# Optimization experiments

Measured on AMD Instinct MI355X. Metric: run time of the kernel, lower is better.

The kernel has to match this reference:

```python
import jax, jax.numpy as jnp
import numpy as np

B, I, O = 4096, 2048, 2048
U_R, THR_MIN = 0.01, 0.01


def setup_inputs() -> dict:
    key = jax.random.key(0)
    ks = jax.random.split(key, 4)
    # Random small-scale weights (the module's ones-init saturates sigmoids;
    # math is identical, this just keeps values in a testable range).
    return {
        "x_t": jax.random.normal(ks[0], (B, I), jnp.float32),
        "u_t": jnp.zeros((B, O), jnp.float32),
        "b_t": jnp.zeros((B, O), jnp.float32),
        "spk": jnp.zeros((B, O), jnp.float32),
        "W_syn": jax.random.normal(ks[1], (O, I), jnp.float32) * 0.02,
        "b_syn": jnp.zeros((O,), jnp.float32),
        "W_Tm": jax.random.normal(ks[2], (O, O), jnp.float32) * 0.02,
        "b_Tm": jnp.zeros((O,), jnp.float32),
        "W_Tadp": jax.random.normal(ks[3], (O, O), jnp.float32) * 0.02,
        "b_Tadp": jnp.zeros((O,), jnp.float32),
    }


def reference(x_t, u_t, b_t, spk, W_syn, b_syn, W_Tm, b_Tm, W_Tadp, b_Tadp):
    # L1 = syn(x_t); Linear stores weight [out,in]
    L1 = x_t @ W_syn.T + b_syn                      # [B, O]
    alpha = jax.nn.sigmoid((L1 + u_t) @ W_Tm.T + b_Tm)
    rho = jax.nn.sigmoid((L1 + b_t) @ W_Tadp.T + b_Tadp)
    b_new = rho * b_t + (1.0 - rho) * spk
    thr = THR_MIN + 1.8 * b_new
    u_new = u_t + (-u_t + L1) / alpha
    o_spk = (u_new - thr > 0).astype(jnp.float32)
    # (state u_t would be reset via o_spk, but forward returns only spikes)
    return o_spk
```

## Files before the change

kernel.cpp:

```cpp
#include <hip/hip_runtime.h>
#include <cmath>

#define B_DIM 4096
#define O_DIM 2048
#define I_DIM 2048

typedef _Float16 f16x8 __attribute__((ext_vector_type(8)));
typedef float f32x4 __attribute__((ext_vector_type(4)));
typedef unsigned int uint;
typedef unsigned short ushort;

#define WSCALE   64.0f
#define WDESCALE 0.015625f
#define MBYTE    ((size_t)1024 * 1024)


__device__ __forceinline__ int TP(int r, int s) {
    return r * 16 + (((s ^ ((r >> 1) & 3))) << 2);
}

__device__ __forceinline__ float h2f(ushort u) {
    _Float16 h = __builtin_bit_cast(_Float16, u);
    return (float)h;
}

__device__ __forceinline__ void gload16(const uint* src, uint* lds) {
    __builtin_amdgcn_global_load_lds(
        (const __attribute__((address_space(1))) void*)src,
        (__attribute__((address_space(3))) void*)lds, 16, 0, 0);
}

__device__ __forceinline__ void split8(const float4 a, const float4 b,
                                       uint4& hi, uint4& lo) {
    auto h0 = __builtin_amdgcn_cvt_pkrtz(a.x, a.y);
    auto h1 = __builtin_amdgcn_cvt_pkrtz(a.z, a.w);
    auto h2 = __builtin_amdgcn_cvt_pkrtz(b.x, b.y);
    auto h3 = __builtin_amdgcn_cvt_pkrtz(b.z, b.w);
    auto l0 = __builtin_amdgcn_cvt_pkrtz(a.x - (float)h0[0], a.y - (float)h0[1]);
    auto l1 = __builtin_amdgcn_cvt_pkrtz(a.z - (float)h1[0], a.w - (float)h1[1]);
    auto l2 = __builtin_amdgcn_cvt_pkrtz(b.x - (float)h2[0], b.y - (float)h2[1]);
    auto l3 = __builtin_amdgcn_cvt_pkrtz(b.z - (float)h3[0], b.w - (float)h3[1]);
    hi.x = __builtin_bit_cast(uint, h0); hi.y = __builtin_bit_cast(uint, h1);
    hi.z = __builtin_bit_cast(uint, h2); hi.w = __builtin_bit_cast(uint, h3);
    lo.x = __builtin_bit_cast(uint, l0); lo.y = __builtin_bit_cast(uint, l1);
    lo.z = __builtin_bit_cast(uint, l2); lo.w = __builtin_bit_cast(uint, l3);
}

__device__ __forceinline__ float4 add4(const float4 a, const float4 b) {
    return make_float4(a.x + b.x, a.y + b.y, a.z + b.z, a.w + b.w);
}
__device__ __forceinline__ float4 mul64(const float4 a) {
    return make_float4(a.x * WSCALE, a.y * WSCALE, a.z * WSCALE, a.w * WSCALE);
}
__device__ __forceinline__ void unpack8(const uint4 h, const uint4 l,
                                        float4& f0, float4& f1) {
    f0.x = h2f((ushort)(h.x & 0xffff)) + h2f((ushort)(l.x & 0xffff));
    f0.y = h2f((ushort)(h.x >> 16))    + h2f((ushort)(l.x >> 16));
    f0.z = h2f((ushort)(h.y & 0xffff)) + h2f((ushort)(l.y & 0xffff));
    f0.w = h2f((ushort)(h.y >> 16))    + h2f((ushort)(l.y >> 16));
    f1.x = h2f((ushort)(h.z & 0xffff)) + h2f((ushort)(l.z & 0xffff));
    f1.y = h2f((ushort)(h.z >> 16))    + h2f((ushort)(l.z >> 16));
    f1.z = h2f((ushort)(h.w & 0xffff)) + h2f((ushort)(l.w & 0xffff));
    f1.w = h2f((ushort)(h.w >> 16))    + h2f((ushort)(l.w >> 16));
}

__global__ __launch_bounds__(256)
void prep(const float* __restrict__ x, const float* __restrict__ Wsyn,
          const float* __restrict__ WTm,
          const float* __restrict__ u, const float* __restrict__ b,
          const float* __restrict__ s,
          ushort* __restrict__ Xh, ushort* __restrict__ Xl,
          ushort* __restrict__ Wsh, ushort* __restrict__ Wsl,
          ushort* __restrict__ Mhp, uint* __restrict__ flag, int doX) {
    const uint NX = (uint)((size_t)B_DIM * I_DIM / 8);
    const uint NW = (uint)((size_t)O_DIM * I_DIM / 8);
    const uint NZ = (uint)((size_t)B_DIM * O_DIM / 8);
    const uint nx = doX ? NX : 0;
    const uint total = nx + 2 * NW + NZ;
    const uint stride = gridDim.x * blockDim.x;
    bool nz = false;
    for (uint t = blockIdx.x * blockDim.x + threadIdx.x; t < total; t += stride) {
        if (t < nx) {
            const size_t i = (size_t)t * 8;
            uint4 h, l;
            split8(*(const float4*)(x + i), *(const float4*)(x + i + 4), h, l);
            *(uint4*)(Xh + i) = h; *(uint4*)(Xl + i) = l;
        } else if (t < nx + NW) {
            const size_t i = (size_t)(t - nx) * 8;
            uint4 h, l;
            split8(mul64(*(const float4*)(Wsyn + i)),
                   mul64(*(const float4*)(Wsyn + i + 4)), h, l);
            *(uint4*)(Wsh + i) = h; *(uint4*)(Wsl + i) = l;
        } else if (t < nx + 2 * NW) {
            const size_t i = (size_t)(t - nx - NW) * 8;
            const float4 a = mul64(*(const float4*)(WTm + i));
            const float4 c = mul64(*(const float4*)(WTm + i + 4));
            auto h0 = __builtin_amdgcn_cvt_pkrtz(a.x, a.y);
            auto h1 = __builtin_amdgcn_cvt_pkrtz(a.z, a.w);
            auto h2 = __builtin_amdgcn_cvt_pkrtz(c.x, c.y);
            auto h3 = __builtin_amdgcn_cvt_pkrtz(c.z, c.w);
            uint4 h;
            h.x = __builtin_bit_cast(uint, h0); h.y = __builtin_bit_cast(uint, h1);
            h.z = __builtin_bit_cast(uint, h2); h.w = __builtin_bit_cast(uint, h3);
            *(uint4*)(Mhp + i) = h;
        } else {
            const size_t i = (size_t)(t - nx - 2 * NW) * 8;
            const float4 a0 = *(const float4*)(u + i), a1 = *(const float4*)(u + i + 4);
            const float4 b0 = *(const float4*)(b + i), b1 = *(const float4*)(b + i + 4);
            const float4 c0 = *(const float4*)(s + i), c1 = *(const float4*)(s + i + 4);
            nz |= (a0.x != 0.f) | (a0.y != 0.f) | (a0.z != 0.f) | (a0.w != 0.f);
            nz |= (a1.x != 0.f) | (a1.y != 0.f) | (a1.z != 0.f) | (a1.w != 0.f);
            nz |= (b0.x != 0.f) | (b0.y != 0.f) | (b0.z != 0.f) | (b0.w != 0.f);
            nz |= (b1.x != 0.f) | (b1.y != 0.f) | (b1.z != 0.f) | (b1.w != 0.f);
            nz |= (c0.x != 0.f) | (c0.y != 0.f) | (c0.z != 0.f) | (c0.w != 0.f);
            nz |= (c1.x != 0.f) | (c1.y != 0.f) | (c1.z != 0.f) | (c1.w != 0.f);
        }
    }
    if (nz) atomicOr(flag, 1u);
}

__global__ __launch_bounds__(1024)
void gemm1_d(const ushort* __restrict__ Xh, const ushort* __restrict__ Xl,
             const ushort* __restrict__ Wh, const ushort* __restrict__ Wl,
             const float* __restrict__ bias,
             ushort* __restrict__ Lh, ushort* __restrict__ Ll) {
    __shared__ uint S[3][12288];

    const int tid = threadIdx.x;
    const int lane = tid & 63;
    const int wid = tid >> 6;
    const int wm = wid >> 3;
    const int wn = wid & 7;

    int sid = blockIdx.x;
    sid = (sid & 7) * 32 + (sid >> 3);
    const int bx = sid & 7, by = sid >> 3;
    const int row0 = by * 128, col0 = bx * 256;

    const uint* src[3];
    int dbase[3];
#pragma unroll
    for (int i = 0; i < 3; i++) {
        const int ch = wid * 3 + i;
        const ushort* plane;
        int local, pbase, grow0;
        if (ch < 8)       { plane = Xh; local = ch;      pbase = 0;    grow0 = row0; }
        else if (ch < 16) { plane = Xl; local = ch - 8;  pbase = 2048; grow0 = row0; }
        else if (ch < 32) { plane = Wh; local = ch - 16; pbase = 4096; grow0 = col0; }
        else              { plane = Wl; local = ch - 32; pbase = 8192; grow0 = col0; }
        const int g = local * 64 + lane;
        const int r = g >> 2, q = (g & 3) ^ ((r >> 1) & 3);
        dbase[i] = pbase + local * 256;
        src[i] = (const uint*)plane + (size_t)(grow0 + r) * 1024 + q * 4;
    }

    f32x4 acc[4][2];
#pragma unroll
    for (int i = 0; i < 4; i++)
#pragma unroll
        for (int j = 0; j < 2; j++)
#pragma unroll
            for (int r = 0; r < 4; r++) acc[i][j][r] = 0.0f;

    const int fr = lane & 15;
    const int sl = lane >> 4;
    const int NT = I_DIM / 32;

#pragma unroll
    for (int i = 0; i < 3; i++) gload16(src[i], &S[0][dbase[i]]);
#pragma unroll
    for (int i = 0; i < 3; i++) gload16(src[i] + 16, &S[1][dbase[i]]);

    for (int t = 0; t < NT; t++) {
        if (t + 1 < NT) {
            asm volatile("s_waitcnt vmcnt(3)" ::: "memory");
        } else {
            asm volatile("s_waitcnt vmcnt(0)" ::: "memory");
        }
        asm volatile("s_barrier" ::: "memory");
        if (t + 2 < NT) {
            const int ko = (t + 2) * 16;
            uint* Sd = &S[(t + 2) % 3][0];
#pragma unroll
            for (int i = 0; i < 3; i++) gload16(src[i] + ko, &Sd[dbase[i]]);
        }
        const uint* Sc = &S[t % 3][0];
        f16x8 ah_[4], al_[4], bh_[2], bl_[2];
#pragma unroll
        for (int mi = 0; mi < 4; mi++) {
            const int r = wm * 64 + mi * 16 + fr;
            ah_[mi] = *(const f16x8*)&Sc[TP(r, sl)];
            al_[mi] = *(const f16x8*)&Sc[2048 + TP(r, sl)];
        }
#pragma unroll
        for (int ni = 0; ni < 2; ni++) {
            const int r = wn * 32 + ni * 16 + fr;
            bh_[ni] = *(const f16x8*)&Sc[4096 + TP(r, sl)];
            bl_[ni] = *(const f16x8*)&Sc[8192 + TP(r, sl)];
        }
#pragma unroll
        for (int mi = 0; mi < 4; mi++)
#pragma unroll
            for (int ni = 0; ni < 2; ni++) {
                acc[mi][ni] = __builtin_amdgcn_mfma_f32_16x16x32_f16(ah_[mi], bh_[ni], acc[mi][ni], 0, 0, 0);
                acc[mi][ni] = __builtin_amdgcn_mfma_f32_16x16x32_f16(ah_[mi], bl_[ni], acc[mi][ni], 0, 0, 0);
                acc[mi][ni] = __builtin_amdgcn_mfma_f32_16x16x32_f16(al_[mi], bh_[ni], acc[mi][ni], 0, 0, 0);
            }
    }

#pragma unroll
    for (int ni = 0; ni < 2; ni++) {
        const int col = col0 + wn * 32 + ni * 16 + fr;
        const float bv = bias[col];
#pragma unroll
        for (int mi = 0; mi < 4; mi++) {
            const int rb = row0 + wm * 64 + mi * 16 + ((lane >> 4) << 2);
            float e[4];
#pragma unroll
            for (int r = 0; r < 4; r++) e[r] = acc[mi][ni][r] * WDESCALE + bv;
            auto hp0 = __builtin_amdgcn_cvt_pkrtz(e[0], e[1]);
            auto hp1 = __builtin_amdgcn_cvt_pkrtz(e[2], e[3]);
            auto lp0 = __builtin_amdgcn_cvt_pkrtz(e[0] - (float)hp0[0], e[1] - (float)hp0[1]);
            auto lp1 = __builtin_amdgcn_cvt_pkrtz(e[2] - (float)hp1[0], e[3] - (float)hp1[1]);
            const uint uh0 = __builtin_bit_cast(uint, hp0);
            const uint uh1 = __builtin_bit_cast(uint, hp1);
            const uint ul0 = __builtin_bit_cast(uint, lp0);
            const uint ul1 = __builtin_bit_cast(uint, lp1);
            Lh[(size_t)(rb + 0) * O_DIM + col] = (ushort)(uh0 & 0xffff);
            Lh[(size_t)(rb + 1) * O_DIM + col] = (ushort)(uh0 >> 16);
            Lh[(size_t)(rb + 2) * O_DIM + col] = (ushort)(uh1 & 0xffff);
            Lh[(size_t)(rb + 3) * O_DIM + col] = (ushort)(uh1 >> 16);
            Ll[(size_t)(rb + 0) * O_DIM + col] = (ushort)(ul0 & 0xffff);
            Ll[(size_t)(rb + 1) * O_DIM + col] = (ushort)(ul0 >> 16);
            Ll[(size_t)(rb + 2) * O_DIM + col] = (ushort)(ul1 & 0xffff);
            Ll[(size_t)(rb + 3) * O_DIM + col] = (ushort)(ul1 >> 16);
        }
    }
}

__global__ __launch_bounds__(256)
void gemm1_b(const float* __restrict__ X,
             const ushort* __restrict__ Wh, const ushort* __restrict__ Wl,
             const float* __restrict__ bias,
             ushort* __restrict__ Lh, ushort* __restrict__ Ll) {
    __shared__ uint S[8192];

    const int tid = threadIdx.x;
    const int lane = tid & 63;
    const int wid = tid >> 6;
    const int wm = wid >> 1, wn = wid & 1;

    int sid = blockIdx.x;
    sid = (sid & 7) * 64 + (sid >> 3);
    const int bx = sid & 15, by = sid >> 4;
    const int row0 = by * 128, col0 = bx * 128;

    const int sr = tid >> 1;
    const int kh = (tid & 1) * 16;
    const int s0 = (tid & 1) * 2;
    const float* pA = X + (size_t)(row0 + sr) * I_DIM + kh;

    int r0, q0, r1, q1;
    {
        const int g0 = (wid * 2 + 0) * 64 + lane;
        const int g1 = (wid * 2 + 1) * 64 + lane;
        r0 = g0 >> 2; q0 = (g0 & 3) ^ ((r0 >> 1) & 3);
        r1 = g1 >> 2; q1 = (g1 & 3) ^ ((r1 >> 1) & 3);
    }
    const uint* sWh0 = (const uint*)Wh + (size_t)(col0 + r0) * 1024 + q0 * 4;
    const uint* sWh1 = (const uint*)Wh + (size_t)(col0 + r1) * 1024 + q1 * 4;
    const uint* sWl0 = (const uint*)Wl + (size_t)(col0 + r0) * 1024 + q0 * 4;
    const uint* sWl1 = (const uint*)Wl + (size_t)(col0 + r1) * 1024 + q1 * 4;
    const int c0 = (wid * 2 + 0) << 8;
    const int c1 = (wid * 2 + 1) << 8;

    f32x4 acc[4][4];
#pragma unroll
    for (int i = 0; i < 4; i++)
#pragma unroll
        for (int j = 0; j < 4; j++)
#pragma unroll
            for (int r = 0; r < 4; r++) acc[i][j][r] = 0.0f;

    const int fr = lane & 15;
    const int sl = lane >> 4;
    const int NT = I_DIM / 32;

    float4 a0 = *(const float4*)(pA + 0), a1 = *(const float4*)(pA + 4);
    float4 a2 = *(const float4*)(pA + 8), a3 = *(const float4*)(pA + 12);
    uint4 xh0, xl0, xh1, xl1;
    split8(a0, a1, xh0, xl0);
    split8(a2, a3, xh1, xl1);

    for (int t = 0; t < NT; t++) {
        __syncthreads();
        *(uint4*)&S[TP(sr, s0)] = xh0;         *(uint4*)&S[TP(sr, s0 + 1)] = xh1;
        *(uint4*)&S[2048 + TP(sr, s0)] = xl0;  *(uint4*)&S[2048 + TP(sr, s0 + 1)] = xl1;
        const int ko = t * 16;
        gload16(sWh0 + ko, &S[4096 + c0]);  gload16(sWh1 + ko, &S[4096 + c1]);
        gload16(sWl0 + ko, &S[6144 + c0]);  gload16(sWl1 + ko, &S[6144 + c1]);
        __syncthreads();
        if (t + 1 < NT) {
            const float* nA = pA + (t + 1) * 32;
            a0 = *(const float4*)(nA + 0); a1 = *(const float4*)(nA + 4);
            a2 = *(const float4*)(nA + 8); a3 = *(const float4*)(nA + 12);
        }
        f16x8 ah_[4], al_[4], bh_[4], bl_[4];
#pragma unroll
        for (int mi = 0; mi < 4; mi++) {
            const int r = wm * 64 + mi * 16 + fr;
            ah_[mi] = *(const f16x8*)&S[TP(r, sl)];
            al_[mi] = *(const f16x8*)&S[2048 + TP(r, sl)];
        }
#pragma unroll
        for (int ni = 0; ni < 4; ni++) {
            const int r = wn * 64 + ni * 16 + fr;
            bh_[ni] = *(const f16x8*)&S[4096 + TP(r, sl)];
            bl_[ni] = *(const f16x8*)&S[6144 + TP(r, sl)];
        }
#pragma unroll
        for (int mi = 0; mi < 4; mi++)
#pragma unroll
            for (int ni = 0; ni < 4; ni++) {
                acc[mi][ni] = __builtin_amdgcn_mfma_f32_16x16x32_f16(ah_[mi], bh_[ni], acc[mi][ni], 0, 0, 0);
                acc[mi][ni] = __builtin_amdgcn_mfma_f32_16x16x32_f16(ah_[mi], bl_[ni], acc[mi][ni], 0, 0, 0);
                acc[mi][ni] = __builtin_amdgcn_mfma_f32_16x16x32_f16(al_[mi], bh_[ni], acc[mi][ni], 0, 0, 0);
            }
        if (t + 1 < NT) {
            split8(a0, a1, xh0, xl0);
            split8(a2, a3, xh1, xl1);
        }
    }

    const int fr2 = lane & 15;
#pragma unroll
    for (int ni = 0; ni < 4; ni++) {
        const int col = col0 + wn * 64 + ni * 16 + fr2;
        const float bv = bias[col];
#pragma unroll
        for (int mi = 0; mi < 4; mi++) {
            const int rb = row0 + wm * 64 + mi * 16 + ((lane >> 4) << 2);
            float e[4];
#pragma unroll
            for (int r = 0; r < 4; r++) e[r] = acc[mi][ni][r] * WDESCALE + bv;
            auto hp0 = __builtin_amdgcn_cvt_pkrtz(e[0], e[1]);
            auto hp1 = __builtin_amdgcn_cvt_pkrtz(e[2], e[3]);
            auto lp0 = __builtin_amdgcn_cvt_pkrtz(e[0] - (float)hp0[0], e[1] - (float)hp0[1]);
            auto lp1 = __builtin_amdgcn_cvt_pkrtz(e[2] - (float)hp1[0], e[3] - (float)hp1[1]);
            const uint uh0 = __builtin_bit_cast(uint, hp0);
            const uint uh1 = __builtin_bit_cast(uint, hp1);
            const uint ul0 = __builtin_bit_cast(uint, lp0);
            const uint ul1 = __builtin_bit_cast(uint, lp1);
            Lh[(size_t)(rb + 0) * O_DIM + col] = (ushort)(uh0 & 0xffff);
            Lh[(size_t)(rb + 1) * O_DIM + col] = (ushort)(uh0 >> 16);
            Lh[(size_t)(rb + 2) * O_DIM + col] = (ushort)(uh1 & 0xffff);
            Lh[(size_t)(rb + 3) * O_DIM + col] = (ushort)(uh1 >> 16);
            Ll[(size_t)(rb + 0) * O_DIM + col] = (ushort)(ul0 & 0xffff);
            Ll[(size_t)(rb + 1) * O_DIM + col] = (ushort)(ul0 >> 16);
            Ll[(size_t)(rb + 2) * O_DIM + col] = (ushort)(ul1 & 0xffff);
            Ll[(size_t)(rb + 3) * O_DIM + col] = (ushort)(ul1 >> 16);
        }
    }
}

__global__ __launch_bounds__(256)
void stage2_fast(const ushort* __restrict__ Lhp, const ushort* __restrict__ Llp,
                 const ushort* __restrict__ Mhp,
                 const float* __restrict__ bTm, float* __restrict__ out,
                 const uint* __restrict__ flag,
                 uint* __restrict__ cnt, uint* __restrict__ list, uint cap) {
    if (*flag != 0) return;

    __shared__ uint S[3][4096];

    const int tid = threadIdx.x;
    const int lane = tid & 63;
    const int wid = tid >> 6;
    const int wm = wid >> 1, wn = wid & 1;

    int sid = blockIdx.x;
    sid = (sid & 7) * 64 + (sid >> 3);
    const int bx = sid & 15, by = sid >> 4;
    const int row0 = by * 128, col0 = bx * 128;

    const uint* srcL0; const uint* srcL1; const uint* srcM0; const uint* srcM1;
    {
        const int g0 = (wid * 2 + 0) * 64 + lane;
        const int g1 = (wid * 2 + 1) * 64 + lane;
        const int r0 = g0 >> 2, q0 = (g0 & 3) ^ ((r0 >> 1) & 3);
        const int r1 = g1 >> 2, q1 = (g1 & 3) ^ ((r1 >> 1) & 3);
        srcL0 = (const uint*)Lhp + (size_t)(row0 + r0) * 1024 + q0 * 4;
        srcL1 = (const uint*)Lhp + (size_t)(row0 + r1) * 1024 + q1 * 4;
        srcM0 = (const uint*)Mhp + (size_t)(col0 + r0) * 1024 + q0 * 4;
        srcM1 = (const uint*)Mhp + (size_t)(col0 + r1) * 1024 + q1 * 4;
    }
    const int c0 = (wid * 2 + 0) << 8;
    const int c1 = (wid * 2 + 1) << 8;

    f32x4 acc[4][4];
#pragma unroll
    for (int i = 0; i < 4; i++)
#pragma unroll
        for (int j = 0; j < 4; j++)
#pragma unroll
            for (int r = 0; r < 4; r++) acc[i][j][r] = 0.0f;

    const int fr = lane & 15;
    const int sl = lane >> 4;
    const int NT = O_DIM / 32;

    gload16(srcL0, &S[0][c0]);         gload16(srcL1, &S[0][c1]);
    gload16(srcM0, &S[0][2048 + c0]);  gload16(srcM1, &S[0][2048 + c1]);
    gload16(srcL0 + 16, &S[1][c0]);        gload16(srcL1 + 16, &S[1][c1]);
    gload16(srcM0 + 16, &S[1][2048 + c0]); gload16(srcM1 + 16, &S[1][2048 + c1]);

    for (int t = 0; t < NT; t++) {
        if (t + 1 < NT) {
            asm volatile("s_waitcnt vmcnt(4)" ::: "memory");
        } else {
            asm volatile("s_waitcnt vmcnt(0)" ::: "memory");
        }
        asm volatile("s_barrier" ::: "memory");
        if (t + 2 < NT) {
            const int ko = (t + 2) * 16;
            uint* Sd = &S[(t + 2) % 3][0];
            gload16(srcL0 + ko, &Sd[c0]);         gload16(srcL1 + ko, &Sd[c1]);
            gload16(srcM0 + ko, &Sd[2048 + c0]);  gload16(srcM1 + ko, &Sd[2048 + c1]);
        }
        const uint* Sc = &S[t % 3][0];
        f16x8 lh_[4], mh_[4];
#pragma unroll
        for (int mi = 0; mi < 4; mi++)
            lh_[mi] = *(const f16x8*)&Sc[TP(wm * 64 + mi * 16 + fr, sl)];
#pragma unroll
        for (int ni = 0; ni < 4; ni++)
            mh_[ni] = *(const f16x8*)&Sc[2048 + TP(wn * 64 + ni * 16 + fr, sl)];
#pragma unroll
        for (int mi = 0; mi < 4; mi++)
#pragma unroll
            for (int ni = 0; ni < 4; ni++)
                acc[mi][ni] = __builtin_amdgcn_mfma_f32_16x16x32_f16(lh_[mi], mh_[ni], acc[mi][ni], 0, 0, 0);
    }
    __syncthreads();

    float* Sf = (float*)&S[0][0];
    float bmv[4];
#pragma unroll
    for (int ni = 0; ni < 4; ni++)
        bmv[ni] = bTm[col0 + wn * 64 + ni * 16 + fr];

    const int erow = tid >> 1;
    const int ecg  = tid & 1;

#pragma unroll
    for (int h = 0; h < 2; h++) {
        if (h) __syncthreads();
#pragma unroll
        for (int ni2 = 0; ni2 < 2; ni2++) {
            const int ni = h * 2 + ni2;
#pragma unroll
            for (int mi = 0; mi < 4; mi++) {
                const int rbL = wm * 64 + mi * 16 + ((lane >> 4) << 2);
#pragma unroll
                for (int r = 0; r < 4; r++) {
                    const int row = rbL + r;
                    const int cm = wn * 32 + ni2 * 16 + fr;
                    const int phys = (cm + ((row >> 2) & 3) * 16 + (row & 3) * 4) & 63;
                    Sf[row * 64 + phys] = acc[mi][ni][r] * WDESCALE + bmv[ni];
                }
            }
        }
        __syncthreads();
        const int rsw = ((erow >> 2) & 3) * 16 + (erow & 3) * 4;
        float z[32];
#pragma unroll
        for (int j = 0; j < 8; j++) {
            const int phys = (ecg * 32 + j * 4 + rsw) & 63;
            *(float4*)&z[j * 4] = *(const float4*)&Sf[erow * 64 + phys];
        }
        const int colBase = col0 + ecg * 64 + h * 32;
        const size_t idx0 = (size_t)(row0 + erow) * O_DIM + colBase;
        uint4 lh4[4], ll4[4];
#pragma unroll
        for (int j = 0; j < 4; j++) {
            lh4[j] = ((const uint4*)(Lhp + idx0))[j];
            ll4[j] = ((const uint4*)(Llp + idx0))[j];
        }
        float ov[32];
#pragma unroll
        for (int m = 0; m < 32; m++) {
            const uint hu = ((const uint*)lh4)[m >> 1];
            const uint lu = ((const uint*)ll4)[m >> 1];
            const ushort hs = (m & 1) ? (ushort)(hu >> 16) : (ushort)(hu & 0xffff);
            const ushort ls = (m & 1) ? (ushort)(lu >> 16) : (ushort)(lu & 0xffff);
            const float l1 = h2f(hs) + h2f(ls);
            const float zm = z[m];
            const float ea = expf(-zm);
            const float d = l1 * (1.0f + ea) - 0.01f;
            ov[m] = d > 0.0f ? 1.0f : 0.0f;
            const float tol = 2e-4f + 1e-4f * ea * (1.0f + fabsf(l1));
            if (fabsf(d) < tol) {
                const uint pos = atomicAdd(cnt, 1u);
                if (pos < cap) list[pos] = (uint)(idx0 + m);
            }
        }
#pragma unroll
        for (int j = 0; j < 8; j++)
            *(float4*)(out + idx0 + j * 4) = *(const float4*)&ov[j * 4];
    }
}

__global__ __launch_bounds__(512)
void stage2_slow(const ushort* __restrict__ Lhp, const ushort* __restrict__ Llp,
                 const float* __restrict__ u_t, const float* __restrict__ b_t,
                 const float* __restrict__ spk,
                 const float* __restrict__ WTm, const float* __restrict__ bTm,
                 const float* __restrict__ WTa, const float* __restrict__ bTa,
                 float* __restrict__ out, const uint* __restrict__ flag,
                 uint* __restrict__ cnt, uint* __restrict__ list, uint cap) {
    if (*flag == 0) return;

    __shared__ uint A1h[128][20], A1l[128][20], A2h[128][20], A2l[128][20];
    __shared__ uint Mh[128][20],  Ml[128][20],  Gh[128][20],  Gl[128][20];

    const int tid = threadIdx.x;
    const int lane = tid & 63;
    const int wid = tid >> 6;
    const int wm = wid >> 2;
    const int wn = wid & 3;

    int sid = blockIdx.x;
    sid = (sid & 7) * 64 + (sid >> 3);
    const int bx = sid & 15, by = sid >> 4;
    const int row0 = by * 128, col0 = bx * 128;

    const int srow = tid >> 2;
    const int skb = (tid & 3) * 8;
    const int swc = (tid & 3) * 4;

    const size_t aoff = (size_t)(row0 + srow) * O_DIM + skb;
    const float* pU = u_t + aoff;
    const float* pT = b_t + aoff;
    const float* pM = WTm + (size_t)(col0 + srow) * O_DIM + skb;
    const float* pG = WTa + (size_t)(col0 + srow) * O_DIM + skb;

    f32x4 accM[4][2], accA[4][2];
#pragma unroll
    for (int i = 0; i < 4; i++)
#pragma unroll
        for (int j = 0; j < 2; j++)
#pragma unroll
            for (int r = 0; r < 4; r++) { accM[i][j][r] = 0.0f; accA[i][j][r] = 0.0f; }

    float4 lq0, lq1;
    {
        const uint4 LH = *(const uint4*)(Lhp + aoff);
        const uint4 LL = *(const uint4*)(Llp + aoff);
        unpack8(LH, LL, lq0, lq1);
    }
    float4 uq0 = *(const float4*)(pU + 0), uq1 = *(const float4*)(pU + 4);
    float4 tq0 = *(const float4*)(pT + 0), tq1 = *(const float4*)(pT + 4);
    float4 mq0 = *(const float4*)(pM + 0), mq1 = *(const float4*)(pM + 4);
    float4 gq0 = *(const float4*)(pG + 0), gq1 = *(const float4*)(pG + 4);

    const int fr = lane & 15;
    const int kq = (lane >> 4) * 4;

    for (int t = 0; t < O_DIM / 32; t++) {
        uint4 A1hi, A1lo, A2hi, A2lo, Mhi, Mlo, Ghi, Glo;
        split8(add4(lq0, uq0), add4(lq1, uq1), A1hi, A1lo);
        split8(add4(lq0, tq0), add4(lq1, tq1), A2hi, A2lo);
        split8(mul64(mq0), mul64(mq1), Mhi, Mlo);
        split8(mul64(gq0), mul64(gq1), Ghi, Glo);
        __syncthreads();
        *(uint4*)&A1h[srow][swc] = A1hi;  *(uint4*)&A1l[srow][swc] = A1lo;
        *(uint4*)&A2h[srow][swc] = A2hi;  *(uint4*)&A2l[srow][swc] = A2lo;
        *(uint4*)&Mh[srow][swc]  = Mhi;   *(uint4*)&Ml[srow][swc]  = Mlo;
        *(uint4*)&Gh[srow][swc]  = Ghi;   *(uint4*)&Gl[srow][swc]  = Glo;
        __syncthreads();
        if (t + 1 < O_DIM / 32) {
            const int o = (t + 1) * 32;
            const uint4 LH = *(const uint4*)(Lhp + aoff + o);
            const uint4 LL = *(const uint4*)(Llp + aoff + o);
            unpack8(LH, LL, lq0, lq1);
            uq0 = *(const float4*)(pU + o);  uq1 = *(const float4*)(pU + o + 4);
            tq0 = *(const float4*)(pT + o);  tq1 = *(const float4*)(pT + o + 4);
            mq0 = *(const float4*)(pM + o);  mq1 = *(const float4*)(pM + o + 4);
            gq0 = *(const float4*)(pG + o);  gq1 = *(const float4*)(pG + o + 4);
        }
        {
            f16x8 ah_[4], al_[4], bh_[2], bl_[2];
#pragma unroll
            for (int mi = 0; mi < 4; mi++) {
                const int r = wm * 64 + mi * 16 + fr;
                ah_[mi] = *(const f16x8*)&A1h[r][kq];
                al_[mi] = *(const f16x8*)&A1l[r][kq];
            }
#pragma unroll
            for (int ni = 0; ni < 2; ni++) {
                const int r = wn * 32 + ni * 16 + fr;
                bh_[ni] = *(const f16x8*)&Mh[r][kq];
                bl_[ni] = *(const f16x8*)&Ml[r][kq];
            }
#pragma unroll
            for (int mi = 0; mi < 4; mi++)
#pragma unroll
                for (int ni = 0; ni < 2; ni++) {
                    accM[mi][ni] = __builtin_amdgcn_mfma_f32_16x16x32_f16(ah_[mi], bh_[ni], accM[mi][ni], 0, 0, 0);
                    accM[mi][ni] = __builtin_amdgcn_mfma_f32_16x16x32_f16(ah_[mi], bl_[ni], accM[mi][ni], 0, 0, 0);
                    accM[mi][ni] = __builtin_amdgcn_mfma_f32_16x16x32_f16(al_[mi], bh_[ni], accM[mi][ni], 0, 0, 0);
                }
        }
        {
            f16x8 ah_[4], al_[4], bh_[2], bl_[2];
#pragma unroll
            for (int mi = 0; mi < 4; mi++) {
                const int r = wm * 64 + mi * 16 + fr;
                ah_[mi] = *(const f16x8*)&A2h[r][kq];
                al_[mi] = *(const f16x8*)&A2l[r][kq];
            }
#pragma unroll
            for (int ni = 0; ni < 2; ni++) {
                const int r = wn * 32 + ni * 16 + fr;
                bh_[ni] = *(const f16x8*)&Gh[r][kq];
                bl_[ni] = *(const f16x8*)&Gl[r][kq];
            }
#pragma unroll
            for (int mi = 0; mi < 4; mi++)
#pragma unroll
                for (int ni = 0; ni < 2; ni++) {
                    accA[mi][ni] = __builtin_amdgcn_mfma_f32_16x16x32_f16(ah_[mi], bh_[ni], accA[mi][ni], 0, 0, 0);
                    accA[mi][ni] = __builtin_amdgcn_mfma_f32_16x16x32_f16(ah_[mi], bl_[ni], accA[mi][ni], 0, 0, 0);
                    accA[mi][ni] = __builtin_amdgcn_mfma_f32_16x16x32_f16(al_[mi], bh_[ni], accA[mi][ni], 0, 0, 0);
                }
        }
    }

#pragma unroll
    for (int ni = 0; ni < 2; ni++) {
        const int col = col0 + wn * 32 + ni * 16 + fr;
        const float bm = bTm[col], bg = bTa[col];
#pragma unroll
        for (int mi = 0; mi < 4; mi++) {
            const int rb = row0 + wm * 64 + mi * 16 + ((lane >> 4) << 2);
#pragma unroll
            for (int r = 0; r < 4; r++) {
                const size_t idx = (size_t)(rb + r) * O_DIM + col;
                const float zm = accM[mi][ni][r] * WDESCALE + bm;
                const float za = accA[mi][ni][r] * WDESCALE + bg;
                const float ut = u_t[idx], bt = b_t[idx];
                const float sp = spk[idx];
                const float l1 = h2f(Lhp[idx]) + h2f(Llp[idx]);
                const float ea  = expf(-zm);
                const float rho = 1.0f / (1.0f + expf(-za));
                const float bn  = sp + rho * (bt - sp);
                const float thr = 0.01f + 1.8f * bn;
                const float un  = ut + (l1 - ut) * (1.0f + ea);
                const float d   = un - thr;
                out[idx] = d > 0.0f ? 1.0f : 0.0f;
                const float tol = 2e-4f + 1e-4f * ea * (1.0f + fabsf(l1 - ut))
                                + 2e-4f * fabsf(bt - sp);
                if (fabsf(d) < tol) {
                    const uint pos = atomicAdd(cnt, 1u);
                    if (pos < cap) list[pos] = (uint)idx;
                }
            }
        }
    }
}

__global__ __launch_bounds__(256)
void lsnn_fixup(const ushort* __restrict__ Lhp, const ushort* __restrict__ Llp,
                const float* __restrict__ X, const float* __restrict__ Wsyn,
                const float* __restrict__ bsyn,
                const float* __restrict__ u_t, const float* __restrict__ b_t,
                const float* __restrict__ spk,
                const float* __restrict__ WTm, const float* __restrict__ bTm,
                const float* __restrict__ WTa, const float* __restrict__ bTa,
                const uint* __restrict__ cnt, const uint* __restrict__ list,
                uint cap, float* __restrict__ out) {
    const uint nc = *cnt;
    const uint n = nc < cap ? nc : cap;
    const int lane = threadIdx.x & 63;
    const uint wid = (blockIdx.x * blockDim.x + threadIdx.x) >> 6;
    const uint nw = (gridDim.x * blockDim.x) >> 6;

    for (uint e = wid; e < n; e += nw) {
        const uint idx = list[e];
        const int b = idx >> 11;
        const int o = idx & (O_DIM - 1);

        double l1 = 0.0, zm = 0.0, za = 0.0;
        const float* xr = X + (size_t)b * I_DIM;
        const float* wr = Wsyn + (size_t)o * I_DIM;
        for (int k = lane; k < I_DIM; k += 64)
            l1 = fma((double)xr[k], (double)wr[k], l1);

        const ushort* lhr = Lhp + (size_t)b * O_DIM;
        const ushort* llr = Llp + (size_t)b * O_DIM;
        const float* ur = u_t + (size_t)b * O_DIM;
        const float* tr = b_t + (size_t)b * O_DIM;
        const float* mr = WTm + (size_t)o * O_DIM;
        const float* ar = WTa + (size_t)o * O_DIM;
        for (int k = lane; k < O_DIM; k += 64) {
            const double l = (double)(h2f(lhr[k]) + h2f(llr[k]));
            zm = fma(l + (double)ur[k], (double)mr[k], zm);
            za = fma(l + (double)tr[k], (double)ar[k], za);
        }
#pragma unroll
        for (int off = 32; off > 0; off >>= 1) {
            l1 += __shfl_down(l1, off);
            zm += __shfl_down(zm, off);
            za += __shfl_down(za, off);
        }
        if (lane == 0) {
            l1 += (double)bsyn[o];
            zm += (double)bTm[o];
            za += (double)bTa[o];
            const double inv_alpha = 1.0 + exp(-zm);
            const double rho = 1.0 / (1.0 + exp(-za));
            const double bt = (double)b_t[idx];
            const double sp = (double)spk[idx];
            const double ut = (double)u_t[idx];
            const double b_new = sp + rho * (bt - sp);
            const double thr = 0.01 + 1.8 * b_new;
            const double u_new = ut + (l1 - ut) * inv_alpha;
            out[idx] = (u_new - thr > 0.0) ? 1.0f : 0.0f;
        }
    }
}

extern "C" void kernel_launch(void* const* d_in, const int* in_sizes, int n_in,
                              void* d_out, int out_size, void* d_ws, size_t ws_size,
                              hipStream_t stream) {
    const float* x    = (const float*)d_in[0];
    const float* u_t  = (const float*)d_in[1];
    const float* b_t  = (const float*)d_in[2];
    const float* spk  = (const float*)d_in[3];
    const float* Wsyn = (const float*)d_in[4];
    const float* bsyn = (const float*)d_in[5];
    const float* WTm  = (const float*)d_in[6];
    const float* bTm  = (const float*)d_in[7];
    const float* WTa  = (const float*)d_in[8];
    const float* bTa  = (const float*)d_in[9];
    float* out = (float*)d_out;

    char* ws = (char*)d_ws;
    ushort* Lhp = (ushort*)(ws + 0 * MBYTE);
    ushort* Llp = (ushort*)(ws + 16 * MBYTE);
    ushort* Mhp = (ushort*)(ws + 32 * MBYTE);
    ushort* Wsh = (ushort*)(ws + 40 * MBYTE);
    ushort* Wsl = (ushort*)(ws + 48 * MBYTE);

    const bool tierA = ws_size >= 91 * MBYTE;
    const size_t flag_off = tierA ? 88 * MBYTE : 56 * MBYTE;
    if (ws_size < flag_off + (1u << 16)) return;

    ushort* Xh = (ushort*)(ws + 56 * MBYTE);
    ushort* Xl = (ushort*)(ws + 72 * MBYTE);
    uint* flag = (uint*)(ws + flag_off);
    uint* cnt  = (uint*)(ws + flag_off + 4);
    uint* list = (uint*)(ws + flag_off + 256);
    const uint cap = (uint)((ws_size - flag_off - 256) / sizeof(uint));

    (void)hipMemsetAsync(ws + flag_off, 0, 8, stream);
    prep<<<dim3(2048), dim3(256), 0, stream>>>(x, Wsyn, WTm, u_t, b_t, spk,
                                               Xh, Xl, Wsh, Wsl, Mhp, flag,
                                               tierA ? 1 : 0);
    if (tierA) {
        gemm1_d<<<dim3(256), dim3(1024), 0, stream>>>(Xh, Xl, Wsh, Wsl, bsyn, Lhp, Llp);
    } else {
        gemm1_b<<<dim3(256), dim3(256), 0, stream>>>(x, Wsh, Wsl, bsyn, Lhp, Llp);
    }
    stage2_fast<<<dim3(512), dim3(256), 0, stream>>>(Lhp, Llp, Mhp, bTm,
                                                     out, flag, cnt, list, cap);
    stage2_slow<<<dim3(512), dim3(512), 0, stream>>>(Lhp, Llp, u_t, b_t, spk,
                                                     WTm, bTm, WTa, bTa,
                                                     out, flag, cnt, list, cap);
    lsnn_fixup<<<dim3(256), dim3(256), 0, stream>>>(Lhp, Llp, x, Wsyn, bsyn,
                                                    u_t, b_t, spk,
                                                    WTm, bTm, WTa, bTa,
                                                    cnt, list, cap, out);
}
```

Before: 249.2 us.

## Double stage2_fast waves per block and raise MFMA priority in GEMM loops

stage2_fast goes from 4 to 8 waves per block. Each wave now computes a 64x32 tile, so its accumulators and B fragments are halved, and the global-to-LDS loads and epilogue are redistributed across the larger block. s_setprio(1) is wrapped around the MFMA sequences in both gemm1 and stage2_fast, so matrix issue is favored over other waves' memory work. The aim is more latency hiding and better overlap of loads with compute. The cost is that each wave issues more LDS reads of the A operand per MFMA, and each block uses more registers.

```diff
diff --git a/kernel.cpp b/kernel.cpp
--- a/kernel.cpp
+++ b/kernel.cpp
@@ -198,6 +198,7 @@
             bh_[ni] = *(const f16x8*)&Sc[4096 + TP(r, sl)];
             bl_[ni] = *(const f16x8*)&Sc[8192 + TP(r, sl)];
         }
+        __builtin_amdgcn_s_setprio(1);
 #pragma unroll
         for (int mi = 0; mi < 4; mi++)
 #pragma unroll
@@ -206,6 +207,7 @@
                 acc[mi][ni] = __builtin_amdgcn_mfma_f32_16x16x32_f16(ah_[mi], bl_[ni], acc[mi][ni], 0, 0, 0);
                 acc[mi][ni] = __builtin_amdgcn_mfma_f32_16x16x32_f16(al_[mi], bh_[ni], acc[mi][ni], 0, 0, 0);
             }
+        __builtin_amdgcn_s_setprio(0);
     }
 
 #pragma unroll
@@ -363,7 +365,7 @@
     }
 }
 
-__global__ __launch_bounds__(256)
+__global__ __launch_bounds__(512)
 void stage2_fast(const ushort* __restrict__ Lhp, const ushort* __restrict__ Llp,
                  const ushort* __restrict__ Mhp,
                  const float* __restrict__ bTm, float* __restrict__ out,
@@ -376,32 +378,37 @@
     const int tid = threadIdx.x;
     const int lane = tid & 63;
     const int wid = tid >> 6;
-    const int wm = wid >> 1, wn = wid & 1;
+    const int wm = wid >> 2;
+    const int wn = wid & 3;
 
     int sid = blockIdx.x;
     sid = (sid & 7) * 64 + (sid >> 3);
     const int bx = sid & 15, by = sid >> 4;
     const int row0 = by * 128, col0 = bx * 128;
 
-    const uint* srcL0; const uint* srcL1; const uint* srcM0; const uint* srcM1;
-    {
-        const int g0 = (wid * 2 + 0) * 64 + lane;
-        const int g1 = (wid * 2 + 1) * 64 + lane;
-        const int r0 = g0 >> 2, q0 = (g0 & 3) ^ ((r0 >> 1) & 3);
-        const int r1 = g1 >> 2, q1 = (g1 & 3) ^ ((r1 >> 1) & 3);
-        srcL0 = (const uint*)Lhp + (size_t)(row0 + r0) * 1024 + q0 * 4;
-        srcL1 = (const uint*)Lhp + (size_t)(row0 + r1) * 1024 + q1 * 4;
-        srcM0 = (const uint*)Mhp + (size_t)(col0 + r0) * 1024 + q0 * 4;
-        srcM1 = (const uint*)Mhp + (size_t)(col0 + r1) * 1024 + q1 * 4;
-    }
-    const int c0 = (wid * 2 + 0) << 8;
-    const int c1 = (wid * 2 + 1) << 8;
-
-    f32x4 acc[4][4];
+    const uint* src[2];
+    int base[2];
+#pragma unroll
+    for (int i = 0; i < 2; i++) {
+        const int ch = wid * 2 + i;
+        if (ch < 8) {
+            const int g = ch * 64 + lane;
+            const int r = g >> 2, q = (g & 3) ^ ((r >> 1) & 3);
+            base[i] = ch * 256;
+            src[i] = (const uint*)Lhp + (size_t)(row0 + r) * 1024 + q * 4;
+        } else {
+            const int g = (ch - 8) * 64 + lane;
+            const int r = g >> 2, q = (g & 3) ^ ((r >> 1) & 3);
+            base[i] = 2048 + (ch - 8) * 256;
+            src[i] = (const uint*)Mhp + (size_t)(col0 + r) * 1024 + q * 4;
+        }
+    }
+
+    f32x4 acc[4][2];
 #pragma unroll
     for (int i = 0; i < 4; i++)
 #pragma unroll
-        for (int j = 0; j < 4; j++)
+        for (int j = 0; j < 2; j++)
 #pragma unroll
             for (int r = 0; r < 4; r++) acc[i][j][r] = 0.0f;
 
@@ -409,14 +416,14 @@
     const int sl = lane >> 4;
     const int NT = O_DIM / 32;
 
-    gload16(srcL0, &S[0][c0]);         gload16(srcL1, &S[0][c1]);
-    gload16(srcM0, &S[0][2048 + c0]);  gload16(srcM1, &S[0][2048 + c1]);
-    gload16(srcL0 + 16, &S[1][c0]);        gload16(srcL1 + 16, &S[1][c1]);
-    gload16(srcM0 + 16, &S[1][2048 + c0]); gload16(srcM1 + 16, &S[1][2048 + c1]);
+#pragma unroll
+    for (int i = 0; i < 2; i++) gload16(src[i], &S[0][base[i]]);
+#pragma unroll
+    for (int i = 0; i < 2; i++) gload16(src[i] + 16, &S[1][base[i]]);
 
     for (int t = 0; t < NT; t++) {
         if (t + 1 < NT) {
-            asm volatile("s_waitcnt vmcnt(4)" ::: "memory");
+            asm volatile("s_waitcnt vmcnt(2)" ::: "memory");
         } else {
             asm volatile("s_waitcnt vmcnt(0)" ::: "memory");
         }
@@ -424,71 +431,75 @@
         if (t + 2 < NT) {
             const int ko = (t + 2) * 16;
             uint* Sd = &S[(t + 2) % 3][0];
-            gload16(srcL0 + ko, &Sd[c0]);         gload16(srcL1 + ko, &Sd[c1]);
-            gload16(srcM0 + ko, &Sd[2048 + c0]);  gload16(srcM1 + ko, &Sd[2048 + c1]);
+#pragma unroll
+            for (int i = 0; i < 2; i++) gload16(src[i] + ko, &Sd[base[i]]);
         }
         const uint* Sc = &S[t % 3][0];
-        f16x8 lh_[4], mh_[4];
+        f16x8 lh_[4], mh_[2];
 #pragma unroll
         for (int mi = 0; mi < 4; mi++)
             lh_[mi] = *(const f16x8*)&Sc[TP(wm * 64 + mi * 16 + fr, sl)];
 #pragma unroll
-        for (int ni = 0; ni < 4; ni++)
-            mh_[ni] = *(const f16x8*)&Sc[2048 + TP(wn * 64 + ni * 16 + fr, sl)];
+        for (int ni = 0; ni < 2; ni++)
+            mh_[ni] = *(const f16x8*)&Sc[2048 + TP(wn * 32 + ni * 16 + fr, sl)];
+        __builtin_amdgcn_s_setprio(1);
 #pragma unroll
         for (int mi = 0; mi < 4; mi++)
 #pragma unroll
-            for (int ni = 0; ni < 4; ni++)
+            for (int ni = 0; ni < 2; ni++)
                 acc[mi][ni] = __builtin_amdgcn_mfma_f32_16x16x32_f16(lh_[mi], mh_[ni], acc[mi][ni], 0, 0, 0);
+        __builtin_amdgcn_s_setprio(0);
     }
     __syncthreads();
 
     float* Sf = (float*)&S[0][0];
-    float bmv[4];
-#pragma unroll
-    for (int ni = 0; ni < 4; ni++)
-        bmv[ni] = bTm[col0 + wn * 64 + ni * 16 + fr];
-
-    const int erow = tid >> 1;
-    const int ecg  = tid & 1;
+    float bmv[2];
+#pragma unroll
+    for (int ni = 0; ni < 2; ni++)
+        bmv[ni] = bTm[col0 + wn * 32 + ni * 16 + fr];
+
+    const int erow = tid >> 2;
+    const int ecg  = tid & 3;
 
 #pragma unroll
     for (int h = 0; h < 2; h++) {
         if (h) __syncthreads();
-#pragma unroll
-        for (int ni2 = 0; ni2 < 2; ni2++) {
-            const int ni = h * 2 + ni2;
-#pragma unroll
-            for (int mi = 0; mi < 4; mi++) {
-                const int rbL = wm * 64 + mi * 16 + ((lane >> 4) << 2);
-#pragma unroll
-                for (int r = 0; r < 4; r++) {
-                    const int row = rbL + r;
-                    const int cm = wn * 32 + ni2 * 16 + fr;
-                    const int phys = (cm + ((row >> 2) & 3) * 16 + (row & 3) * 4) & 63;
-                    Sf[row * 64 + phys] = acc[mi][ni][r] * WDESCALE + bmv[ni];
+        if ((wn >> 1) == h) {
+            const int cm0 = (wn & 1) * 32;
+#pragma unroll
+            for (int ni = 0; ni < 2; ni++) {
+#pragma unroll
+                for (int mi = 0; mi < 4; mi++) {
+                    const int rbL = wm * 64 + mi * 16 + ((lane >> 4) << 2);
+#pragma unroll
+                    for (int r = 0; r < 4; r++) {
+                        const int row = rbL + r;
+                        const int cm = cm0 + ni * 16 + fr;
+                        const int phys = (cm + ((row >> 2) & 3) * 16 + (row & 3) * 4) & 63;
+                        Sf[row * 64 + phys] = acc[mi][ni][r] * WDESCALE + bmv[ni];
+                    }
                 }
             }
         }
         __syncthreads();
         const int rsw = ((erow >> 2) & 3) * 16 + (erow & 3) * 4;
-        float z[32];
-#pragma unroll
-        for (int j = 0; j < 8; j++) {
-            const int phys = (ecg * 32 + j * 4 + rsw) & 63;
+        float z[16];
+#pragma unroll
+        for (int j = 0; j < 4; j++) {
+            const int phys = (ecg * 16 + j * 4 + rsw) & 63;
             *(float4*)&z[j * 4] = *(const float4*)&Sf[erow * 64 + phys];
         }
-        const int colBase = col0 + ecg * 64 + h * 32;
+        const int colBase = col0 + h * 64 + ecg * 16;
         const size_t idx0 = (size_t)(row0 + erow) * O_DIM + colBase;
-        uint4 lh4[4], ll4[4];
-#pragma unroll
-        for (int j = 0; j < 4; j++) {
+        uint4 lh4[2], ll4[2];
+#pragma unroll
+        for (int j = 0; j < 2; j++) {
             lh4[j] = ((const uint4*)(Lhp + idx0))[j];
             ll4[j] = ((const uint4*)(Llp + idx0))[j];
         }
-        float ov[32];
-#pragma unroll
-        for (int m = 0; m < 32; m++) {
+        float ov[16];
+#pragma unroll
+        for (int m = 0; m < 16; m++) {
             const uint hu = ((const uint*)lh4)[m >> 1];
             const uint lu = ((const uint*)ll4)[m >> 1];
             const ushort hs = (m & 1) ? (ushort)(hu >> 16) : (ushort)(hu & 0xffff);
@@ -505,7 +516,7 @@
             }
         }
 #pragma unroll
-        for (int j = 0; j < 8; j++)
+        for (int j = 0; j < 4; j++)
             *(float4*)(out + idx0 + j * 4) = *(const float4*)&ov[j * 4];
     }
 }
@@ -772,7 +783,7 @@
     } else {
         gemm1_b<<<dim3(256), dim3(256), 0, stream>>>(x, Wsh, Wsl, bsyn, Lhp, Llp);
     }
-    stage2_fast<<<dim3(512), dim3(256), 0, stream>>>(Lhp, Llp, Mhp, bTm,
+    stage2_fast<<<dim3(512), dim3(512), 0, stream>>>(Lhp, Llp, Mhp, bTm,
                                                      out, flag, cnt, list, cap);
     stage2_slow<<<dim3(512), dim3(512), 0, stream>>>(Lhp, Llp, u_t, b_t, spk,
                                                      WTm, bTm, WTa, bTa,
```

New measurement: 239.8 us. 3.8% less time.
